# Kernel tuning notes

Hardware: AMD Instinct MI355X
Metric: run time of the kernel (lower is better)

Reference implementation:

```python
import jax, jax.numpy as jnp
import numpy as np

N = 50000   # nodes
E = 800000  # edges
H = 4       # num_heads
D = 32      # out_dim
IN = 256    # in_dim


def setup_inputs() -> dict:
    key = jax.random.key(0)
    k0, k1, k2, k3, k4, k5 = jax.random.split(key, 6)
    h = jax.random.normal(k0, (N, IN), dtype=jnp.float32)
    # fl weight (torch Linear stores [out, in]), xavier-ish scale
    Wl = jax.random.normal(k1, (H * D, IN), dtype=jnp.float32) * (1.0 / np.sqrt(IN))
    # fc / fq are initialized to small constants in torch; use small random here
    fc = jax.random.normal(k2, (IN, H * D), dtype=jnp.float32) * 0.02
    fq = jax.random.normal(k3, (IN, H * D), dtype=jnp.float32) * 0.02
    src = jax.random.randint(k4, (E,), 0, N)
    dst = jax.random.randint(k5, (E,), 0, N)
    return {"h": h, "Wl": Wl, "fc": fc, "fq": fq, "src": src, "dst": dst}


def reference(h, Wl, fc, fq, src, dst):
    n = h.shape[0]
    ft = (h @ Wl.T).reshape(n, H, D)      # [N,H,D]
    ft_c = (h @ fc).reshape(n, H, D)      # [N,H,D]
    ft_q = (h @ fq).reshape(n, H, D)      # [N,H,D]

    # edge attention: c = ft_c[dst], q = ft_q[src] - c, a = ELU(sum(q*c))
    c = ft_c[dst]                         # [E,H,D]
    a = jax.nn.elu(jnp.sum((ft_q[src] - c) * c, axis=-1))  # [E,H]

    # segmented (per-destination) softmax over incoming edges, per head
    m = jax.ops.segment_max(a, dst, num_segments=n)        # [N,H]
    ex = jnp.exp(a - m[dst])
    s = jax.ops.segment_sum(ex, dst, num_segments=n)       # [N,H]
    attn = ex / s[dst]                                     # [E,H]

    # global top-k (smallest l_s) threshold + mass redistribution, per head
    l_s = int(0.713 * attn.shape[0])
    srt = jnp.sort(attn, axis=0)                           # ascending per head
    thd = srt[l_s - 1]                                     # [H] l_s-th smallest
    topk_sum = jnp.sum(srt[:l_s], axis=0)                  # [H]
    a2 = jnp.where(attn - thd < 0, jnp.zeros((), attn.dtype), attn)
    ratio = (jnp.sum(a2, axis=0) + topk_sum) / jnp.sum(a2, axis=0)  # [H]
    a3 = a2 * ratio                                        # [E,H]

    # weighted scatter-sum of source features to destinations
    out = jax.ops.segment_sum(ft[src] * a3[:, :, None], dst, num_segments=n)  # [N,H,D]

    # concat=True: cat(flattened heads, mean over heads of ft)
    return jnp.concatenate([out.reshape(n, -1), ft.mean(axis=1)], axis=1)  # [N, H*D + D]
```

## Files before the change

### kernel.cpp

```cpp
#include <hip/hip_runtime.h>
#include <hip/hip_bf16.h>
#include <math.h>

#define N_NODES 50000
#define N_EDGES 800000
#define DH 32
#define IN_DIM 256
#define OUTC 160
#define LS 570400
#define RANK0 (LS - 1)
#define DEG_CAP 160
#define BCAP 65536
#define MARG 3.0e-4

typedef unsigned long long u64;
#define SC_FX 1099511627776.0
#define SC_32 4294967296.0

__global__ void k_deg(const int* __restrict__ dst, unsigned* __restrict__ A){
  int e = blockIdx.x * 256 + threadIdx.x;
  if (e < N_EDGES) atomicAdd(&A[dst[e]], 1u);
}

__global__ __launch_bounds__(1024) void k_scan(unsigned* __restrict__ A){
  __shared__ unsigned ps[1024];
  int t = threadIdx.x;
  const int CH = (N_NODES + 1023) / 1024;
  int base = t * CH;
  unsigned s = 0;
  for (int i = 0; i < CH; i++){ int n = base + i; if (n < N_NODES) s += A[n]; }
  ps[t] = s;
  __syncthreads();
  for (int off = 1; off < 1024; off <<= 1){
    unsigned v = (t >= off) ? ps[t - off] : 0;
    __syncthreads();
    ps[t] += v;
    __syncthreads();
  }
  unsigned ex = (t == 0) ? 0 : ps[t - 1];
  for (int i = 0; i < CH; i++){
    int n = base + i;
    if (n < N_NODES){ unsigned dv = A[n]; A[n] = ex; ex += dv; }
  }
}

__global__ void k_fill(const int* __restrict__ dst, unsigned* __restrict__ A,
                       unsigned* __restrict__ eidx){
  int e = blockIdx.x * 256 + threadIdx.x;
  if (e < N_EDGES) eidx[atomicAdd(&A[dst[e]], 1u)] = (unsigned)e;
}

__global__ void k_init(unsigned* __restrict__ sel32, unsigned* __restrict__ krem,
                       unsigned* __restrict__ cnt, unsigned* __restrict__ done,
                       unsigned* __restrict__ ccnt, unsigned* __restrict__ cbelow,
                       unsigned* __restrict__ bcnt, unsigned* __restrict__ cntless,
                       u64* __restrict__ gsums){
  int t = threadIdx.x;
  if (t < 4){ sel32[t]=0; krem[t]=RANK0; cnt[t]=0; ccnt[t]=0; cbelow[t]=0; cntless[t]=0; }
  if (t < 8) gsums[t] = 0;
  if (t == 0){ done[0] = 0; bcnt[0] = 0; }
}

__global__ void k_prept(const float* __restrict__ fc, const float* __restrict__ fq,
                        float* __restrict__ fcT, float* __restrict__ fqT){
  int i = blockIdx.x * 256 + threadIdx.x;
  if (i >= IN_DIM * 128) return;
  int k = i >> 7, c = i & 127;
  fcT[(size_t)c * 256 + k] = fc[i];
  fqT[(size_t)c * 256 + k] = fq[i];
}

#define BM 128
#define BK 16
__global__ __launch_bounds__(256) void k_gemm384(const float* __restrict__ A,
    const float* __restrict__ Wl, const float* __restrict__ fc,
    const float* __restrict__ fq, float* __restrict__ C){
  __shared__ float As[2][BK][BM + 4];
  __shared__ float Bs[2][BK][128 + 4];
  int tid = threadIdx.x;
  int m0 = blockIdx.x * BM;
  int n0 = blockIdx.y * 128;
  int ty = tid / 16, tx = tid % 16;
  const float* Bsrc = (n0 == 128) ? fc : fq;

  int sA0r = (tid * 2) >> 2,     sA0c = (tid * 2) & 3;
  int sA1r = (tid * 2 + 1) >> 2, sA1c = (tid * 2 + 1) & 3;
  int sB0k = (tid * 2) >> 5,     sB0c = (tid * 2) & 31;
  int sB1k = (tid * 2 + 1) >> 5, sB1c = (tid * 2 + 1) & 31;

  float acc[8][8];
  #pragma unroll
  for (int i = 0; i < 8; i++)
    #pragma unroll
    for (int j = 0; j < 8; j++) acc[i][j] = 0.f;

  float4 rA0, rA1, rB0, rB1;
  {
    int r0 = m0 + sA0r, r1 = m0 + sA1r;
    rA0 = (r0 < N_NODES) ? *(const float4*)&A[(size_t)r0 * IN_DIM + sA0c * 4] : make_float4(0,0,0,0);
    rA1 = (r1 < N_NODES) ? *(const float4*)&A[(size_t)r1 * IN_DIM + sA1c * 4] : make_float4(0,0,0,0);
    if (n0 == 0){
      rB0 = *(const float4*)&Wl[(size_t)sA0r * IN_DIM + sA0c * 4];
      rB1 = *(const float4*)&Wl[(size_t)sA1r * IN_DIM + sA1c * 4];
    } else {
      rB0 = *(const float4*)&Bsrc[(size_t)sB0k * 128 + sB0c * 4];
      rB1 = *(const float4*)&Bsrc[(size_t)sB1k * 128 + sB1c * 4];
    }
  }

  int p = 0;
  for (int k0 = 0; k0 < IN_DIM; k0 += BK){
    As[p][sA0c * 4 + 0][sA0r] = rA0.x; As[p][sA0c * 4 + 1][sA0r] = rA0.y;
    As[p][sA0c * 4 + 2][sA0r] = rA0.z; As[p][sA0c * 4 + 3][sA0r] = rA0.w;
    As[p][sA1c * 4 + 0][sA1r] = rA1.x; As[p][sA1c * 4 + 1][sA1r] = rA1.y;
    As[p][sA1c * 4 + 2][sA1r] = rA1.z; As[p][sA1c * 4 + 3][sA1r] = rA1.w;
    if (n0 == 0){
      Bs[p][sA0c * 4 + 0][sA0r] = rB0.x; Bs[p][sA0c * 4 + 1][sA0r] = rB0.y;
      Bs[p][sA0c * 4 + 2][sA0r] = rB0.z; Bs[p][sA0c * 4 + 3][sA0r] = rB0.w;
      Bs[p][sA1c * 4 + 0][sA1r] = rB1.x; Bs[p][sA1c * 4 + 1][sA1r] = rB1.y;
      Bs[p][sA1c * 4 + 2][sA1r] = rB1.z; Bs[p][sA1c * 4 + 3][sA1r] = rB1.w;
    } else {
      *(float4*)&Bs[p][sB0k][sB0c * 4] = rB0;
      *(float4*)&Bs[p][sB1k][sB1c * 4] = rB1;
    }
    __syncthreads();
    if (k0 + BK < IN_DIM){
      int kn = k0 + BK;
      int r0 = m0 + sA0r, r1 = m0 + sA1r;
      rA0 = (r0 < N_NODES) ? *(const float4*)&A[(size_t)r0 * IN_DIM + kn + sA0c * 4] : make_float4(0,0,0,0);
      rA1 = (r1 < N_NODES) ? *(const float4*)&A[(size_t)r1 * IN_DIM + kn + sA1c * 4] : make_float4(0,0,0,0);
      if (n0 == 0){
        rB0 = *(const float4*)&Wl[(size_t)sA0r * IN_DIM + kn + sA0c * 4];
        rB1 = *(const float4*)&Wl[(size_t)sA1r * IN_DIM + kn + sA1c * 4];
      } else {
        rB0 = *(const float4*)&Bsrc[(size_t)(kn + sB0k) * 128 + sB0c * 4];
        rB1 = *(const float4*)&Bsrc[(size_t)(kn + sB1k) * 128 + sB1c * 4];
      }
    }
    #pragma unroll
    for (int kk = 0; kk < BK; kk++){
      float4 a0 = *(const float4*)&As[p][kk][ty * 4];
      float4 a1 = *(const float4*)&As[p][kk][64 + ty * 4];
      float4 b0 = *(const float4*)&Bs[p][kk][tx * 4];
      float4 b1 = *(const float4*)&Bs[p][kk][64 + tx * 4];
      float av[8] = {a0.x, a0.y, a0.z, a0.w, a1.x, a1.y, a1.z, a1.w};
      float bv[8] = {b0.x, b0.y, b0.z, b0.w, b1.x, b1.y, b1.z, b1.w};
      #pragma unroll
      for (int i = 0; i < 8; i++)
        #pragma unroll
        for (int j = 0; j < 8; j++)
          acc[i][j] = fmaf(av[i], bv[j], acc[i][j]);
    }
    p ^= 1;
  }
  #pragma unroll
  for (int i = 0; i < 8; i++){
    int r = m0 + ((i < 4) ? (ty * 4 + i) : (64 + ty * 4 + (i - 4)));
    if (r >= N_NODES) continue;
    *(float4*)&C[(size_t)r * 384 + n0 + tx * 4]      = make_float4(acc[i][0], acc[i][1], acc[i][2], acc[i][3]);
    *(float4*)&C[(size_t)r * 384 + n0 + 64 + tx * 4] = make_float4(acc[i][4], acc[i][5], acc[i][6], acc[i][7]);
  }
}

__global__ __launch_bounds__(256) void k_softedge32(const float* __restrict__ fcq,
    const int* __restrict__ src, const unsigned* __restrict__ A,
    const unsigned* __restrict__ eidx, float* __restrict__ abuf){
  __shared__ float lds_a[8][DEG_CAP * 4];
  int tid = threadIdx.x;
  int wv = tid >> 6;
  int l = tid & 63;
  int half = l >> 5;
  int ll = l & 31;
  int ds = wv * 2 + half;
  int d = blockIdx.x * 8 + ds;
  bool ok = (d < N_NODES);
  unsigned k0 = 0, k1 = 0;
  if (ok){ k0 = d ? A[d - 1] : 0u; k1 = A[d]; }
  unsigned deg = k1 - k0;
  float4 c4 = make_float4(0.f, 0.f, 0.f, 0.f);
  float4 q4n = make_float4(0.f, 0.f, 0.f, 0.f);
  if (deg){
    c4 = *(const float4*)&fcq[(size_t)d * 384 + 128 + ll * 4];
    int sn = src[eidx[k0]];
    q4n = *(const float4*)&fcq[(size_t)sn * 384 + 256 + ll * 4];
  }
  float m = -1.0e30f;
  for (unsigned kk = 0; kk < deg; kk++){
    float4 q4 = q4n;
    if (kk + 1 < deg){
      int s2 = src[eidx[k0 + kk + 1]];
      q4n = *(const float4*)&fcq[(size_t)s2 * 384 + 256 + ll * 4];
    }
    float v = (q4.x - c4.x) * c4.x;
    v = fmaf(q4.y - c4.y, c4.y, v);
    v = fmaf(q4.z - c4.z, c4.z, v);
    v = fmaf(q4.w - c4.w, c4.w, v);
    v += __shfl_xor(v, 1);
    v += __shfl_xor(v, 2);
    v += __shfl_xor(v, 4);
    float a = (v > 0.f) ? v : expm1f(v);
    m = fmaxf(m, a);
    if ((ll & 7) == 0) lds_a[ds][kk * 4 + (ll >> 3)] = a;
  }
  float mm = __shfl(m, half * 32 + (ll & 3) * 8);
  unsigned nj = deg * 4;
  long long sfx = 0;
  for (unsigned jj = ll; jj < nj; jj += 32){
    float ex = __expf(lds_a[ds][jj] - mm);
    lds_a[ds][jj] = ex;
    sfx += (long long)llrintf(ex * (float)SC_32);
  }
  sfx += __shfl_xor(sfx, 4);
  sfx += __shfl_xor(sfx, 8);
  sfx += __shfl_xor(sfx, 16);
  if (deg){
    float sd = (float)((double)sfx * (1.0 / SC_32));
    for (unsigned jj = ll; jj < nj; jj += 32)
      abuf[(size_t)k0 * 4 + jj] = lds_a[ds][jj] / sd;
  }
}

__global__ __launch_bounds__(256) void k_hp32(const float* __restrict__ attn,
    unsigned* __restrict__ sel32, unsigned* __restrict__ krem, unsigned* __restrict__ cnt,
    unsigned* __restrict__ hist, unsigned* __restrict__ done, unsigned maskHi, int shift){
  __shared__ unsigned lh[1024];
  __shared__ unsigned ticket;
  for (int j = threadIdx.x; j < 1024; j += 256) lh[j] = 0;
  __syncthreads();
  int i0 = blockIdx.x * 256 + threadIdx.x;
  int hh = i0 & 3;
  unsigned sel = sel32[hh] & maskHi;
  const int total = N_EDGES * 4;
  for (int i = i0; i < total; i += gridDim.x * 256){
    unsigned u = __float_as_uint(attn[i]);
    if ((u & maskHi) == sel)
      atomicAdd(&lh[hh * 256 + ((u >> shift) & 255u)], 1u);
  }
  __syncthreads();
  for (int j = threadIdx.x; j < 1024; j += 256)
    if (lh[j]) atomicAdd(&hist[j], lh[j]);
  __threadfence();
  if (threadIdx.x == 0) ticket = atomicAdd(done, 1u);
  __syncthreads();
  if (ticket == gridDim.x - 1){
    __threadfence();
    for (int j = threadIdx.x; j < 1024; j += 256){ lh[j] = hist[j]; hist[j] = 0; }
    __syncthreads();
    if (threadIdx.x < 4){
      int t = threadIdx.x;
      unsigned kr = krem[t], cum = 0, b = 0;
      for (; b < 256; b++){
        unsigned c2 = lh[t * 256 + b];
        if (kr < cum + c2) break;
        cum += c2;
      }
      sel32[t] |= b << shift;
      krem[t] = kr - cum;
      cnt[t] += cum;
    }
    if (threadIdx.x == 0) *done = 0;
  }
}

__global__ __launch_bounds__(256) void k_compact32(const float* __restrict__ attn,
    const unsigned* __restrict__ sel32, unsigned* __restrict__ ccnt,
    float* __restrict__ cand){
  __shared__ unsigned lcnt[4];
  __shared__ unsigned lbase[4];
  int t = threadIdx.x;
  if (t < 4) lcnt[t] = 0;
  __syncthreads();
  int i0 = blockIdx.x * 256 + t;
  int hh = i0 & 3;
  unsigned sel = sel32[hh] & 0xFFFF0000u;
  const int total = N_EDGES * 4;
  unsigned mc = 0;
  for (int i = i0; i < total; i += gridDim.x * 256){
    unsigned u = __float_as_uint(attn[i]);
    if ((u & 0xFFFF0000u) == sel) mc++;
  }
  unsigned my_local = mc ? atomicAdd(&lcnt[hh], mc) : 0u;
  __syncthreads();
  if (t < 4) lbase[t] = lcnt[t] ? atomicAdd(&ccnt[t], lcnt[t]) : 0u;
  __syncthreads();
  if (mc == 0) return;
  unsigned pos = lbase[hh] + my_local;
  float* cp = cand + (size_t)hh * N_EDGES;
  for (int i = i0; i < total; i += gridDim.x * 256){
    float v = attn[i];
    unsigned u = __float_as_uint(v);
    if ((u & 0xFFFF0000u) == sel) cp[pos++] = v;
  }
}

__global__ __launch_bounds__(256) void k_fin32(const float* __restrict__ cand,
    const unsigned* __restrict__ ccnt, unsigned* __restrict__ sel32,
    unsigned* __restrict__ krem, unsigned* __restrict__ cnt,
    unsigned* __restrict__ hist, unsigned* __restrict__ done, int shift){
  __shared__ unsigned lh[256];
  __shared__ unsigned ticket;
  int t = threadIdx.x;
  lh[t] = 0;
  __syncthreads();
  int h = blockIdx.x & 3;
  int bidx = blockIdx.x >> 2;
  int bph = gridDim.x >> 2;
  unsigned maskHi = ~((1u << (shift + 8)) - 1u);
  unsigned sel = sel32[h] & maskHi;
  unsigned n = ccnt[h];
  const float* cp = cand + (size_t)h * N_EDGES;
  for (unsigned i = bidx * 256 + t; i < n; i += bph * 256){
    unsigned u = __float_as_uint(cp[i]);
    if ((u & maskHi) == sel) atomicAdd(&lh[(u >> shift) & 255u], 1u);
  }
  __syncthreads();
  if (lh[t]) atomicAdd(&hist[h * 256 + t], lh[t]);
  __threadfence();
  if (t == 0) ticket = atomicAdd(done, 1u);
  __syncthreads();
  if (ticket == gridDim.x - 1){
    __threadfence();
    __shared__ unsigned fh[1024];
    for (int j = t; j < 1024; j += 256){ fh[j] = hist[j]; hist[j] = 0; }
    __syncthreads();
    if (t < 4){
      unsigned kr = krem[t], cum = 0, b = 0;
      for (; b < 256; b++){
        unsigned c2 = fh[t * 256 + b];
        if (kr < cum + c2) break;
        cum += c2;
      }
      sel32[t] |= b << shift;
      krem[t] = kr - cum;
      cnt[t] += cum;
    }
    if (t == 0) *done = 0;
  }
}

__global__ __launch_bounds__(256) void k_marksums(const float* __restrict__ attn,
    const unsigned* __restrict__ sel32, unsigned* __restrict__ cbelow,
    unsigned* __restrict__ bcnt, unsigned* __restrict__ blist,
    u64* __restrict__ gsums, float* __restrict__ a3){
  int t = threadIdx.x;
  int i0 = blockIdx.x * 256 + t;
  int hh = t & 3;
  double thd = (double)__uint_as_float(sel32[hh]);
  double lo = thd * (1.0 - MARG), hi = thd * (1.0 + MARG);
  double al = 0.0, ag = 0.0;
  unsigned below = 0;
  const int total = N_EDGES * 4;
  for (int i = i0; i < total; i += gridDim.x * 256){
    float vf = attn[i];
    double v = (double)vf;
    if (v < lo){ al += v; below++; a3[i] = 0.f; }
    else if (v > hi){ ag += v; a3[i] = vf; }
    else {
      unsigned p = atomicAdd(bcnt, 1u);
      if (p < BCAP) blist[p] = (unsigned)i;
      a3[i] = 0.f;
    }
  }
  long long ql = llrint(al * SC_FX);
  long long qg = llrint(ag * SC_FX);
  #pragma unroll
  for (int m = 4; m < 64; m <<= 1){
    ql += __shfl_xor(ql, m);
    qg += __shfl_xor(qg, m);
    below += __shfl_xor(below, m);
  }
  __shared__ long long sl[16], sg[16];
  __shared__ unsigned sb[16];
  int wv = t >> 6;
  if ((t & 63) < 4){ sl[wv * 4 + hh] = ql; sg[wv * 4 + hh] = qg; sb[wv * 4 + hh] = below; }
  __syncthreads();
  if (t < 4){
    long long a = sl[t] + sl[4 + t] + sl[8 + t] + sl[12 + t];
    long long b = sg[t] + sg[4 + t] + sg[8 + t] + sg[12 + t];
    unsigned bl = sb[t] + sb[4 + t] + sb[8 + t] + sb[12 + t];
    if (a) atomicAdd(&gsums[t],     (u64)a);
    if (b) atomicAdd(&gsums[4 + t], (u64)b);
    if (bl) atomicAdd(&cbelow[t], bl);
  }
}

__global__ __launch_bounds__(256) void k_brefine(const float* __restrict__ h,
    const float* __restrict__ fcT, const float* __restrict__ fqT,
    const int* __restrict__ src, const int* __restrict__ dst,
    const unsigned* __restrict__ A, const unsigned* __restrict__ eidx,
    const unsigned* __restrict__ blist, const unsigned* __restrict__ bcnt,
    double* __restrict__ bval){
  __shared__ float wqs[32][257];
  __shared__ double cs[32];
  __shared__ double la[DEG_CAP];
  int tid = threadIdx.x;
  int wv = tid >> 6;
  int l = tid & 63;
  int j = l & 31;
  int khalf = l >> 5;
  unsigned nb = *bcnt; if (nb > BCAP) nb = BCAP;
  for (unsigned idx = blockIdx.x; idx < nb; idx += gridDim.x){
    unsigned slot = blist[idx];
    unsigned kslot = slot >> 2;
    int hh = slot & 3;
    int d = dst[eidx[kslot]];
    unsigned k0 = d ? A[d - 1] : 0u, k1 = A[d];
    unsigned deg = k1 - k0;
    {
      int col = tid >> 3, seg = tid & 7;
      const float* gsrc = fqT + (size_t)(hh * 32 + col) * 256 + seg * 32;
      #pragma unroll
      for (int r = 0; r < 8; r++){
        float4 v = *(const float4*)&gsrc[r * 4];
        float* wdst = &wqs[col][seg * 32 + r * 4];
        wdst[0] = v.x; wdst[1] = v.y; wdst[2] = v.z; wdst[3] = v.w;
      }
    }
    __syncthreads();
    if (wv == 0){
      const float* hd = h + (size_t)d * 256 + khalf * 128;
      const float* wc = fcT + (size_t)(hh * 32 + j) * 256 + khalf * 128;
      double c0 = 0.0, c1 = 0.0, c2 = 0.0, c3 = 0.0;
      #pragma unroll 8
      for (int i = 0; i < 128; i += 4){
        float4 hv = *(const float4*)&hd[i];
        float4 w2 = *(const float4*)&wc[i];
        c0 = fma((double)hv.x, (double)w2.x, c0);
        c1 = fma((double)hv.y, (double)w2.y, c1);
        c2 = fma((double)hv.z, (double)w2.z, c2);
        c3 = fma((double)hv.w, (double)w2.w, c3);
      }
      double c = (c0 + c1) + (c2 + c3);
      c += __shfl_xor(c, 32);
      if (l < 32) cs[l] = c;
    }
    __syncthreads();
    double cj = cs[j];
    for (unsigned k = k0 + wv; k < k1; k += 4){
      int s = src[eidx[k]];
      const float* hs = h + (size_t)s * 256 + khalf * 128;
      const float* wr = &wqs[j][khalf * 128];
      float4 hv = *(const float4*)&hs[0];
      double q0 = 0.0, q1 = 0.0, q2 = 0.0, q3 = 0.0;
      #pragma unroll 4
      for (int i = 0; i < 128; i += 4){
        float4 cur = hv;
        if (i + 4 < 128) hv = *(const float4*)&hs[i + 4];
        q0 = fma((double)cur.x, (double)wr[i + 0], q0);
        q1 = fma((double)cur.y, (double)wr[i + 1], q1);
        q2 = fma((double)cur.z, (double)wr[i + 2], q2);
        q3 = fma((double)cur.w, (double)wr[i + 3], q3);
      }
      double q = (q0 + q1) + (q2 + q3);
      q += __shfl_xor(q, 32);
      double p = (q - cj) * cj;
      p += __shfl_xor(p, 1);
      p += __shfl_xor(p, 2);
      p += __shfl_xor(p, 4);
      p += __shfl_xor(p, 8);
      p += __shfl_xor(p, 16);
      double a = (p > 0.0) ? p : expm1(p);
      if (l == 0) la[k - k0] = a;
    }
    __syncthreads();
    if (wv == 0){
      double m = -1.0e300;
      for (unsigned kk = l; kk < deg; kk += 64) m = fmax(m, la[kk]);
      #pragma unroll
      for (int msk = 1; msk < 64; msk <<= 1) m = fmax(m, __shfl_xor(m, msk));
      long long sfx = 0;
      for (unsigned kk = l; kk < deg; kk += 64)
        sfx += llrint(exp(la[kk] - m) * SC_FX);
      #pragma unroll
      for (int msk = 1; msk < 64; msk <<= 1) sfx += __shfl_xor(sfx, msk);
      if (l == 0){
        double sd = (double)sfx * (1.0 / SC_FX);
        bval[idx] = exp(la[kslot - k0] - m) / sd;
      }
    }
    __syncthreads();
  }
}

__global__ __launch_bounds__(256) void k_bselect(const double* __restrict__ bval,
    const unsigned* __restrict__ blist, const unsigned* __restrict__ bcnt,
    const unsigned* __restrict__ cbelow, double* __restrict__ thd64,
    unsigned* __restrict__ cntless){
  __shared__ unsigned lh[256];
  __shared__ u64 s_sel;
  __shared__ unsigned s_kr, s_cnt;
  int hsel = blockIdx.x;
  int t = threadIdx.x;
  unsigned nb = *bcnt; if (nb > BCAP) nb = BCAP;
  if (t == 0){ s_sel = 0; s_kr = RANK0 - cbelow[hsel]; s_cnt = 0; }
  __syncthreads();
  for (int p = 0; p < 8; p++){
    int shift = 56 - 8 * p;
    u64 maskHi = (p == 0) ? 0ull : (~0ull) << (64 - 8 * p);
    lh[t] = 0;
    __syncthreads();
    u64 sel = s_sel;
    for (unsigned i = t; i < nb; i += 256){
      if ((int)(blist[i] & 3) == hsel){
        u64 u = (u64)__double_as_longlong(bval[i]);
        if ((u & maskHi) == sel) atomicAdd(&lh[(unsigned)((u >> shift) & 255u)], 1u);
      }
    }
    __syncthreads();
    if (t == 0){
      unsigned kr = s_kr, cum = 0, b = 0;
      for (; b < 256; b++){
        unsigned c2 = lh[b];
        if (kr < cum + c2) break;
        cum += c2;
      }
      s_sel |= ((u64)b) << shift;
      s_kr = kr - cum;
      s_cnt += cum;
    }
    __syncthreads();
  }
  if (t == 0){
    thd64[hsel] = __longlong_as_double((long long)s_sel);
    cntless[hsel] = cbelow[hsel] + s_cnt;
  }
}

__global__ void k_bfinal(const unsigned* __restrict__ blist, const double* __restrict__ bval,
    const unsigned* __restrict__ bcnt, const double* __restrict__ thd64,
    u64* __restrict__ gsums, float* __restrict__ a3){
  unsigned nb = *bcnt; if (nb > BCAP) nb = BCAP;
  for (unsigned idx = blockIdx.x * 256 + threadIdx.x; idx < nb; idx += gridDim.x * 256){
    unsigned slot = blist[idx];
    int hh = slot & 3;
    double v = bval[idx];
    bool kept = (v >= thd64[hh]);
    a3[slot] = kept ? (float)v : 0.f;
    atomicAdd(&gsums[(kept ? 4 : 0) + hh], (u64)llrint(v * SC_FX));
  }
}

__global__ void k_ratio(const double* __restrict__ thd64, const unsigned* __restrict__ cntless,
                        const u64* __restrict__ gsums, double* __restrict__ trd){
  int t = threadIdx.x;
  if (t < 4){
    double sless = (double)(long long)gsums[t]     * (1.0 / SC_FX);
    double sge   = (double)(long long)gsums[4 + t] * (1.0 / SC_FX);
    double topk  = sless + (double)(LS - (int)cntless[t]) * thd64[t];
    trd[t] = thd64[t];
    trd[4 + t] = (sge + topk) / sge;
  }
}

__global__ __launch_bounds__(256) void k_scatter2(const float* __restrict__ fcq,
    const int* __restrict__ src, const unsigned* __restrict__ A,
    const unsigned* __restrict__ eidx, const float* __restrict__ a3,
    const double* __restrict__ trd, float* __restrict__ out){
  int tid = threadIdx.x;
  int wv = tid >> 6;
  int l = tid & 63;
  int half = l >> 5;
  int ll = l & 31;
  int d = blockIdx.x * 8 + wv * 2 + half;
  if (d >= N_NODES) return;
  int hh = ll >> 3;
  double ratio = trd[4 + hh];
  unsigned k0 = d ? A[d - 1] : 0u, k1 = A[d];
  long long acc0 = 0, acc1 = 0, acc2 = 0, acc3 = 0;
  float wn = (k0 < k1) ? a3[(size_t)k0 * 4 + hh] : 0.f;
  unsigned en = (k0 < k1) ? eidx[k0] : 0u;
  for (unsigned k = k0; k < k1; k++){
    float w = wn;
    unsigned e = en;
    if (k + 1 < k1){ wn = a3[(size_t)(k + 1) * 4 + hh]; en = eidx[k + 1]; }
    unsigned hb = (unsigned)(__ballot(w != 0.f) >> (half * 32));
    if (hb == 0u) continue;
    if (w != 0.f){
      int s = src[e];
      float4 f = *(const float4*)&fcq[(size_t)s * 384 + ll * 4];
      double a3r = (double)w * ratio;
      acc0 += llrint(a3r * (double)f.x * SC_FX);
      acc1 += llrint(a3r * (double)f.y * SC_FX);
      acc2 += llrint(a3r * (double)f.z * SC_FX);
      acc3 += llrint(a3r * (double)f.w * SC_FX);
    }
  }
  float* p = &out[(size_t)d * OUTC + ll * 4];
  p[0] = (float)((double)acc0 * (1.0 / SC_FX));
  p[1] = (float)((double)acc1 * (1.0 / SC_FX));
  p[2] = (float)((double)acc2 * (1.0 / SC_FX));
  p[3] = (float)((double)acc3 * (1.0 / SC_FX));
  const float* pf = &fcq[(size_t)d * 384];
  out[(size_t)d * OUTC + 128 + ll] = 0.25f * (pf[ll] + pf[32 + ll] + pf[64 + ll] + pf[96 + ll]);
}

extern "C" void kernel_launch(void* const* d_in, const int* in_sizes, int n_in,
                              void* d_out, int out_size, void* d_ws, size_t ws_size,
                              hipStream_t stream){
  const float* h  = (const float*)d_in[0];
  const float* Wl = (const float*)d_in[1];
  const float* fc = (const float*)d_in[2];
  const float* fq = (const float*)d_in[3];
  const int* src  = (const int*)d_in[4];
  const int* dst  = (const int*)d_in[5];
  float* out = (float*)d_out;

  char* ws = (char*)d_ws;
  float*    fcq  = (float*)(ws);
  unsigned* A    = (unsigned*)(ws + 76800000);
  unsigned* eidx = (unsigned*)(ws + 77000064);
  float*    a3   = (float*)(ws + 80200064);
  unsigned* hist = (unsigned*)(ws + 93000064);
  unsigned* sel32  = (unsigned*)(ws + 93004160);
  unsigned* krem   = (unsigned*)(ws + 93004176);
  unsigned* cnt    = (unsigned*)(ws + 93004192);
  unsigned* done   = (unsigned*)(ws + 93004208);
  unsigned* ccnt   = (unsigned*)(ws + 93004224);
  unsigned* cbelow = (unsigned*)(ws + 93004240);
  unsigned* bcnt   = (unsigned*)(ws + 93004256);
  unsigned* cntless= (unsigned*)(ws + 93004272);
  u64*      gsums  = (u64*)(ws + 93004288);
  double*   thd64  = (double*)(ws + 93004352);
  double*   trd    = (double*)(ws + 93004416);
  unsigned* blist  = (unsigned*)(ws + 93008896);
  double*   bval   = (double*)(ws + 93271040);
  float*    fcT    = (float*)(ws + 93795328);
  float*    fqT    = (float*)(ws + 93926400);

  float* abuf = (float*)d_out;
  float* cand = (float*)((char*)d_out + 12800000);

  hipMemsetAsync(A, 0, 200004, stream);
  hipMemsetAsync(hist, 0, 4096, stream);
  k_init<<<1, 64, 0, stream>>>(sel32, krem, cnt, done, ccnt, cbelow, bcnt, cntless, gsums);
  k_prept<<<(IN_DIM * 128 + 255) / 256, 256, 0, stream>>>(fc, fq, fcT, fqT);

  k_deg<<<(N_EDGES + 255) / 256, 256, 0, stream>>>(dst, A);
  k_scan<<<1, 1024, 0, stream>>>(A);
  k_fill<<<(N_EDGES + 255) / 256, 256, 0, stream>>>(dst, A, eidx);

  dim3 gg((N_NODES + BM - 1) / BM, 3);
  k_gemm384<<<gg, 256, 0, stream>>>(h, Wl, fc, fq, fcq);

  k_softedge32<<<(N_NODES + 7) / 8, 256, 0, stream>>>(fcq, src, A, eidx, abuf);

  k_hp32<<<1024, 256, 0, stream>>>(abuf, sel32, krem, cnt, hist, done, 0u, 24);
  k_hp32<<<1024, 256, 0, stream>>>(abuf, sel32, krem, cnt, hist, done, 0xFF000000u, 16);
  k_compact32<<<1024, 256, 0, stream>>>(abuf, sel32, ccnt, cand);
  k_fin32<<<256, 256, 0, stream>>>(cand, ccnt, sel32, krem, cnt, hist, done, 8);
  k_fin32<<<256, 256, 0, stream>>>(cand, ccnt, sel32, krem, cnt, hist, done, 0);

  k_marksums<<<2048, 256, 0, stream>>>(abuf, sel32, cbelow, bcnt, blist, gsums, a3);

  k_brefine<<<2048, 256, 0, stream>>>(h, fcT, fqT, src, dst, A, eidx, blist, bcnt, bval);
  k_bselect<<<4, 256, 0, stream>>>(bval, blist, bcnt, cbelow, thd64, cntless);
  k_bfinal<<<64, 256, 0, stream>>>(blist, bval, bcnt, thd64, gsums, a3);
  k_ratio<<<1, 64, 0, stream>>>(thd64, cntless, gsums, trd);

  k_scatter2<<<(N_NODES + 7) / 8, 256, 0, stream>>>(fcq, src, A, eidx, a3, trd, out);
}
```

Before: 918.4 us.

## Merge init/memset/transpose launches, fuse boundary select-final-ratio, halve GEMM BK

The two memsets, the init kernel and the fc/fq transpose are folded into one init kernel. The boundary select, final fixup and ratio kernels become a single per-head kernel that reduces sums in-block instead of with global atomics. The GEMM K-tile drops from 16 to 8 with one float4 load per thread per operand. This cuts launch count and tiny-kernel overhead, but the GEMM now synchronizes twice as often with less work per stage.

Result: no change. 905.7 us (median of 2 runs) (-1.4%).

```diff
diff --git a/kernel.cpp b/kernel.cpp
--- a/kernel.cpp
+++ b/kernel.cpp
@@ -50,28 +50,28 @@
   if (e < N_EDGES) eidx[atomicAdd(&A[dst[e]], 1u)] = (unsigned)e;
 }
 
-__global__ void k_init(unsigned* __restrict__ sel32, unsigned* __restrict__ krem,
-                       unsigned* __restrict__ cnt, unsigned* __restrict__ done,
-                       unsigned* __restrict__ ccnt, unsigned* __restrict__ cbelow,
-                       unsigned* __restrict__ bcnt, unsigned* __restrict__ cntless,
-                       u64* __restrict__ gsums){
-  int t = threadIdx.x;
-  if (t < 4){ sel32[t]=0; krem[t]=RANK0; cnt[t]=0; ccnt[t]=0; cbelow[t]=0; cntless[t]=0; }
-  if (t < 8) gsums[t] = 0;
-  if (t == 0){ done[0] = 0; bcnt[0] = 0; }
-}
-
-__global__ void k_prept(const float* __restrict__ fc, const float* __restrict__ fq,
-                        float* __restrict__ fcT, float* __restrict__ fqT){
-  int i = blockIdx.x * 256 + threadIdx.x;
-  if (i >= IN_DIM * 128) return;
-  int k = i >> 7, c = i & 127;
-  fcT[(size_t)c * 256 + k] = fc[i];
-  fqT[(size_t)c * 256 + k] = fq[i];
+__global__ void k_init2(unsigned* __restrict__ A, unsigned* __restrict__ hist,
+    unsigned* __restrict__ sel32, unsigned* __restrict__ krem,
+    unsigned* __restrict__ cnt, unsigned* __restrict__ done,
+    unsigned* __restrict__ ccnt, unsigned* __restrict__ cbelow,
+    unsigned* __restrict__ bcnt, u64* __restrict__ gsums,
+    const float* __restrict__ fc, const float* __restrict__ fq,
+    float* __restrict__ fcT, float* __restrict__ fqT){
+  int gid = blockIdx.x * 256 + threadIdx.x;
+  if (gid <= N_NODES) A[gid] = 0;
+  if (gid < 1024) hist[gid] = 0;
+  if (gid < 4){ sel32[gid]=0; krem[gid]=RANK0; cnt[gid]=0; ccnt[gid]=0; cbelow[gid]=0; }
+  if (gid < 8) gsums[gid] = 0;
+  if (gid == 0){ done[0] = 0; bcnt[0] = 0; }
+  if (gid < IN_DIM * 128){
+    int k = gid >> 7, c = gid & 127;
+    fcT[(size_t)c * 256 + k] = fc[gid];
+    fqT[(size_t)c * 256 + k] = fq[gid];
+  }
 }
 
 #define BM 128
-#define BK 16
+#define BK 8
 __global__ __launch_bounds__(256) void k_gemm384(const float* __restrict__ A,
     const float* __restrict__ Wl, const float* __restrict__ fc,
     const float* __restrict__ fq, float* __restrict__ C){
@@ -83,10 +83,8 @@
   int ty = tid / 16, tx = tid % 16;
   const float* Bsrc = (n0 == 128) ? fc : fq;
 
-  int sA0r = (tid * 2) >> 2,     sA0c = (tid * 2) & 3;
-  int sA1r = (tid * 2 + 1) >> 2, sA1c = (tid * 2 + 1) & 3;
-  int sB0k = (tid * 2) >> 5,     sB0c = (tid * 2) & 31;
-  int sB1k = (tid * 2 + 1) >> 5, sB1c = (tid * 2 + 1) & 31;
+  int aR = tid >> 1, aC = tid & 1;
+  int bK = tid >> 5, bC = tid & 31;
 
   float acc[8][8];
   #pragma unroll
@@ -94,48 +92,31 @@
     #pragma unroll
     for (int j = 0; j < 8; j++) acc[i][j] = 0.f;
 
-  float4 rA0, rA1, rB0, rB1;
+  float4 rA, rB;
   {
-    int r0 = m0 + sA0r, r1 = m0 + sA1r;
-    rA0 = (r0 < N_NODES) ? *(const float4*)&A[(size_t)r0 * IN_DIM + sA0c * 4] : make_float4(0,0,0,0);
-    rA1 = (r1 < N_NODES) ? *(const float4*)&A[(size_t)r1 * IN_DIM + sA1c * 4] : make_float4(0,0,0,0);
-    if (n0 == 0){
-      rB0 = *(const float4*)&Wl[(size_t)sA0r * IN_DIM + sA0c * 4];
-      rB1 = *(const float4*)&Wl[(size_t)sA1r * IN_DIM + sA1c * 4];
-    } else {
-      rB0 = *(const float4*)&Bsrc[(size_t)sB0k * 128 + sB0c * 4];
-      rB1 = *(const float4*)&Bsrc[(size_t)sB1k * 128 + sB1c * 4];
-    }
+    int r0 = m0 + aR;
+    rA = (r0 < N_NODES) ? *(const float4*)&A[(size_t)r0 * IN_DIM + aC * 4] : make_float4(0,0,0,0);
+    rB = (n0 == 0) ? *(const float4*)&Wl[(size_t)aR * IN_DIM + aC * 4]
+                   : *(const float4*)&Bsrc[(size_t)bK * 128 + bC * 4];
   }
 
   int p = 0;
   for (int k0 = 0; k0 < IN_DIM; k0 += BK){
-    As[p][sA0c * 4 + 0][sA0r] = rA0.x; As[p][sA0c * 4 + 1][sA0r] = rA0.y;
-    As[p][sA0c * 4 + 2][sA0r] = rA0.z; As[p][sA0c * 4 + 3][sA0r] = rA0.w;
-    As[p][sA1c * 4 + 0][sA1r] = rA1.x; As[p][sA1c * 4 + 1][sA1r] = rA1.y;
-    As[p][sA1c * 4 + 2][sA1r] = rA1.z; As[p][sA1c * 4 + 3][sA1r] = rA1.w;
+    As[p][aC * 4 + 0][aR] = rA.x; As[p][aC * 4 + 1][aR] = rA.y;
+    As[p][aC * 4 + 2][aR] = rA.z; As[p][aC * 4 + 3][aR] = rA.w;
     if (n0 == 0){
-      Bs[p][sA0c * 4 + 0][sA0r] = rB0.x; Bs[p][sA0c * 4 + 1][sA0r] = rB0.y;
-      Bs[p][sA0c * 4 + 2][sA0r] = rB0.z; Bs[p][sA0c * 4 + 3][sA0r] = rB0.w;
-      Bs[p][sA1c * 4 + 0][sA1r] = rB1.x; Bs[p][sA1c * 4 + 1][sA1r] = rB1.y;
-      Bs[p][sA1c * 4 + 2][sA1r] = rB1.z; Bs[p][sA1c * 4 + 3][sA1r] = rB1.w;
+      Bs[p][aC * 4 + 0][aR] = rB.x; Bs[p][aC * 4 + 1][aR] = rB.y;
+      Bs[p][aC * 4 + 2][aR] = rB.z; Bs[p][aC * 4 + 3][aR] = rB.w;
     } else {
-      *(float4*)&Bs[p][sB0k][sB0c * 4] = rB0;
-      *(float4*)&Bs[p][sB1k][sB1c * 4] = rB1;
+      *(float4*)&Bs[p][bK][bC * 4] = rB;
     }
     __syncthreads();
     if (k0 + BK < IN_DIM){
       int kn = k0 + BK;
-      int r0 = m0 + sA0r, r1 = m0 + sA1r;
-      rA0 = (r0 < N_NODES) ? *(const float4*)&A[(size_t)r0 * IN_DIM + kn + sA0c * 4] : make_float4(0,0,0,0);
-      rA1 = (r1 < N_NODES) ? *(const float4*)&A[(size_t)r1 * IN_DIM + kn + sA1c * 4] : make_float4(0,0,0,0);
-      if (n0 == 0){
-        rB0 = *(const float4*)&Wl[(size_t)sA0r * IN_DIM + kn + sA0c * 4];
-        rB1 = *(const float4*)&Wl[(size_t)sA1r * IN_DIM + kn + sA1c * 4];
-      } else {
-        rB0 = *(const float4*)&Bsrc[(size_t)(kn + sB0k) * 128 + sB0c * 4];
-        rB1 = *(const float4*)&Bsrc[(size_t)(kn + sB1k) * 128 + sB1c * 4];
-      }
+      int r0 = m0 + aR;
+      rA = (r0 < N_NODES) ? *(const float4*)&A[(size_t)r0 * IN_DIM + kn + aC * 4] : make_float4(0,0,0,0);
+      rB = (n0 == 0) ? *(const float4*)&Wl[(size_t)aR * IN_DIM + kn + aC * 4]
+                     : *(const float4*)&Bsrc[(size_t)(kn + bK) * 128 + bC * 4];
     }
     #pragma unroll
     for (int kk = 0; kk < BK; kk++){
@@ -482,13 +463,14 @@
   }
 }
 
-__global__ __launch_bounds__(256) void k_bselect(const double* __restrict__ bval,
+__global__ __launch_bounds__(256) void k_bfr(const double* __restrict__ bval,
     const unsigned* __restrict__ blist, const unsigned* __restrict__ bcnt,
-    const unsigned* __restrict__ cbelow, double* __restrict__ thd64,
-    unsigned* __restrict__ cntless){
+    const unsigned* __restrict__ cbelow, const u64* __restrict__ gsums,
+    float* __restrict__ a3, double* __restrict__ trd){
   __shared__ unsigned lh[256];
   __shared__ u64 s_sel;
   __shared__ unsigned s_kr, s_cnt;
+  __shared__ long long sl[4], sg[4];
   int hsel = blockIdx.x;
   int t = threadIdx.x;
   unsigned nb = *bcnt; if (nb > BCAP) nb = BCAP;
@@ -520,35 +502,35 @@
     }
     __syncthreads();
   }
+  double thd = __longlong_as_double((long long)s_sel);
+  long long ql = 0, qg = 0;
+  for (unsigned idx = t; idx < nb; idx += 256){
+    unsigned slot = blist[idx];
+    if ((int)(slot & 3) == hsel){
+      double v = bval[idx];
+      bool kept = (v >= thd);
+      a3[slot] = kept ? (float)v : 0.f;
+      long long q = llrint(v * SC_FX);
+      if (kept) qg += q; else ql += q;
+    }
+  }
+  #pragma unroll
+  for (int msk = 1; msk < 64; msk <<= 1){
+    ql += __shfl_xor(ql, msk);
+    qg += __shfl_xor(qg, msk);
+  }
+  int wv = t >> 6;
+  if ((t & 63) == 0){ sl[wv] = ql; sg[wv] = qg; }
+  __syncthreads();
   if (t == 0){
-    thd64[hsel] = __longlong_as_double((long long)s_sel);
-    cntless[hsel] = cbelow[hsel] + s_cnt;
-  }
-}
-
-__global__ void k_bfinal(const unsigned* __restrict__ blist, const double* __restrict__ bval,
-    const unsigned* __restrict__ bcnt, const double* __restrict__ thd64,
-    u64* __restrict__ gsums, float* __restrict__ a3){
-  unsigned nb = *bcnt; if (nb > BCAP) nb = BCAP;
-  for (unsigned idx = blockIdx.x * 256 + threadIdx.x; idx < nb; idx += gridDim.x * 256){
-    unsigned slot = blist[idx];
-    int hh = slot & 3;
-    double v = bval[idx];
-    bool kept = (v >= thd64[hh]);
-    a3[slot] = kept ? (float)v : 0.f;
-    atomicAdd(&gsums[(kept ? 4 : 0) + hh], (u64)llrint(v * SC_FX));
-  }
-}
-
-__global__ void k_ratio(const double* __restrict__ thd64, const unsigned* __restrict__ cntless,
-                        const u64* __restrict__ gsums, double* __restrict__ trd){
-  int t = threadIdx.x;
-  if (t < 4){
-    double sless = (double)(long long)gsums[t]     * (1.0 / SC_FX);
-    double sge   = (double)(long long)gsums[4 + t] * (1.0 / SC_FX);
-    double topk  = sless + (double)(LS - (int)cntless[t]) * thd64[t];
-    trd[t] = thd64[t];
-    trd[4 + t] = (sge + topk) / sge;
+    long long bl = sl[0] + sl[1] + sl[2] + sl[3];
+    long long bg = sg[0] + sg[1] + sg[2] + sg[3];
+    double sless = (double)((long long)gsums[hsel]     + bl) * (1.0 / SC_FX);
+    double sge   = (double)((long long)gsums[4 + hsel] + bg) * (1.0 / SC_FX);
+    unsigned cl = cbelow[hsel] + s_cnt;
+    double topk = sless + (double)(LS - (int)cl) * thd;
+    trd[hsel] = thd;
+    trd[4 + hsel] = (sge + topk) / sge;
   }
 }
 
@@ -618,9 +600,7 @@
   unsigned* ccnt   = (unsigned*)(ws + 93004224);
   unsigned* cbelow = (unsigned*)(ws + 93004240);
   unsigned* bcnt   = (unsigned*)(ws + 93004256);
-  unsigned* cntless= (unsigned*)(ws + 93004272);
   u64*      gsums  = (u64*)(ws + 93004288);
-  double*   thd64  = (double*)(ws + 93004352);
   double*   trd    = (double*)(ws + 93004416);
   unsigned* blist  = (unsigned*)(ws + 93008896);
   double*   bval   = (double*)(ws + 93271040);
@@ -630,10 +610,8 @@
   float* abuf = (float*)d_out;
   float* cand = (float*)((char*)d_out + 12800000);
 
-  hipMemsetAsync(A, 0, 200004, stream);
-  hipMemsetAsync(hist, 0, 4096, stream);
-  k_init<<<1, 64, 0, stream>>>(sel32, krem, cnt, done, ccnt, cbelow, bcnt, cntless, gsums);
-  k_prept<<<(IN_DIM * 128 + 255) / 256, 256, 0, stream>>>(fc, fq, fcT, fqT);
+  k_init2<<<256, 256, 0, stream>>>(A, hist, sel32, krem, cnt, done, ccnt,
+                                   cbelow, bcnt, gsums, fc, fq, fcT, fqT);
 
   k_deg<<<(N_EDGES + 255) / 256, 256, 0, stream>>>(dst, A);
   k_scan<<<1, 1024, 0, stream>>>(A);
@@ -653,9 +631,7 @@
   k_marksums<<<2048, 256, 0, stream>>>(abuf, sel32, cbelow, bcnt, blist, gsums, a3);
 
   k_brefine<<<2048, 256, 0, stream>>>(h, fcT, fqT, src, dst, A, eidx, blist, bcnt, bval);
-  k_bselect<<<4, 256, 0, stream>>>(bval, blist, bcnt, cbelow, thd64, cntless);
-  k_bfinal<<<64, 256, 0, stream>>>(blist, bval, bcnt, thd64, gsums, a3);
-  k_ratio<<<1, 64, 0, stream>>>(thd64, cntless, gsums, trd);
+  k_bfr<<<4, 256, 0, stream>>>(bval, blist, bcnt, cbelow, gsums, a3, trd);
 
   k_scatter2<<<(N_NODES + 7) / 8, 256, 0, stream>>>(fcq, src, A, eidx, a3, trd, out);
 }
```
